# Kernel tuning notes

Hardware: AMD Instinct MI355X
Metric: run time of the kernel (lower is better)

Reference implementation:

```python
import jax, jax.numpy as jnp
import numpy as np

EPS = 1e-12

def _normalize(v):
    n = jnp.linalg.norm(v, axis=-1, keepdims=True)
    return v / jnp.maximum(n, EPS)

def _bgs(J):
    # J: [b, N, D, 3, 2] -> rotation matrices R [b, N, D, 3, 3]
    b1 = _normalize(J[..., :, 0])
    a2 = J[..., :, 1]
    dot = jnp.sum(b1 * a2, axis=-1, keepdims=True)
    b2 = _normalize(a2 - dot * b1)
    b3 = jnp.cross(b1, b2)
    return jnp.stack([b1, b2, b3], axis=-1)  # columns b1,b2,b3

def setup_inputs() -> dict:
    key = jax.random.key(0)
    k1, k2, k3, k4, k5 = jax.random.split(key, 5)
    B, N, D, OUT = 16, 4096, 64, 64
    X = jax.random.normal(k1, (B, N, D, 3), dtype=jnp.float32)
    J = jax.random.normal(k2, (B, N, D, 3, 2), dtype=jnp.float32)
    A = jax.random.normal(k3, (OUT, D), dtype=jnp.float32)
    Bm = jax.random.normal(k4, (OUT, D), dtype=jnp.float32)
    C = jax.random.normal(k5, (OUT, D), dtype=jnp.float32)
    return {"X": X, "J": J, "A": A, "Bm": Bm, "C": C}

def reference(X, J, A, Bm, C):
    R = _bgs(J)  # [b, N, D, 3, 3]
    # RT_i . X == column i of R dotted with X -> scalar per channel
    RTX = jnp.einsum('bndij,bndi->bndj', R, X)  # [b, N, D, 3], j-th entry = RT_j X
    rt0 = RTX[..., 0:1]
    rt1 = RTX[..., 1:2]
    rt2 = RTX[..., 2:3]
    col0 = R[..., :, 0]
    col1 = R[..., :, 1]
    col2 = R[..., :, 2]
    # a_term (after adding b_term, as in original forward)
    a_term = col1 * rt1 + col2 * rt2 + col2 * rt1 - col1 * rt2  # [b, N, D, 3]
    c_term = col0 * rt0
    Y = jnp.einsum('fe,bnei->bnfi', A, a_term) + jnp.einsum('fe,bnei->bnfi', C, c_term)
    Y = jnp.einsum('fe,bnei->bnfi', Bm, Y)
    return Y
```

## Files before the change

kernel.cpp:

```cpp
#include <hip/hip_runtime.h>


typedef __bf16 bf16x8 __attribute__((ext_vector_type(8)));
typedef float floatx4 __attribute__((ext_vector_type(4)));

#define ZRS  68
#define WLDS 816

__global__ __launch_bounds__(64) void prep_kernel(const float* __restrict__ A,
                                                  const float* __restrict__ Bm,
                                                  const float* __restrict__ C,
                                                  __bf16* __restrict__ acat) {
    int tid = blockIdx.x * 64 + threadIdx.x;
    int f = tid >> 6;
    int e = tid & 63;
    float m = 0.f, m2 = 0.f;
    #pragma unroll 8
    for (int k = 0; k < 64; ++k) {
        float b = Bm[f * 64 + k];
        m  = fmaf(b, A[k * 64 + e], m);
        m2 = fmaf(b, C[k * 64 + e], m2);
    }
    int mt  = f >> 4, l15 = f & 15;
    int k1  = 2 * e;
    int kc  = k1 >> 5;
    int qd  = (k1 >> 3) & 3;
    int j   = k1 & 7;
    int p   = ((mt * 4 + kc) * 64 + qd * 16 + l15) * 8 + j;
    acat[p]     = (__bf16)m;
    acat[p + 1] = (__bf16)m2;
}

static __device__ __forceinline__ unsigned pk(float a, float c) {
    unsigned short ua = __builtin_bit_cast(unsigned short, (__bf16)a);
    unsigned short uc = __builtin_bit_cast(unsigned short, (__bf16)c);
    return ((unsigned)uc << 16) | ua;
}

__global__ __launch_bounds__(256, 5) void main_kernel(const float* __restrict__ X,
                                                      const float* __restrict__ J,
                                                      const __bf16* __restrict__ acat,
                                                      float* __restrict__ out) {
    __shared__ __align__(16) float lds[4096 + 4 * WLDS];

    const int tid  = threadIdx.x;
    const int wave = tid >> 6;
    const int lane = tid & 63;
    const int l15  = lane & 15;
    const int quad = lane >> 4;
    const int pbase = blockIdx.x * 16 + wave * 4;

    const floatx4* ag = (const floatx4*)acat;
    floatx4 t0 = ag[tid];
    floatx4 t1 = ag[256 + tid];
    floatx4 t2 = ag[512 + tid];
    floatx4 t3 = ag[768 + tid];

    float2 jreg[4][3];
    float  xreg[4][3];
    {
        const float* Jb = J + (size_t)pbase * 384 + lane * 6;
        const float* Xb = X + (size_t)pbase * 192 + lane * 3;
        #pragma unroll
        for (int pi = 0; pi < 4; ++pi) {
            jreg[pi][0] = *(const float2*)(Jb + pi * 384);
            jreg[pi][1] = *(const float2*)(Jb + pi * 384 + 2);
            jreg[pi][2] = *(const float2*)(Jb + pi * 384 + 4);
            xreg[pi][0] = Xb[pi * 192];
            xreg[pi][1] = Xb[pi * 192 + 1];
            xreg[pi][2] = Xb[pi * 192 + 2];
        }
    }

    {
        floatx4* al = (floatx4*)lds;
        al[tid]       = t0;
        al[256 + tid] = t1;
        al[512 + tid] = t2;
        al[768 + tid] = t3;
    }

    float* zbase = lds + 4096 + wave * WLDS;

    #pragma unroll
    for (int pi = 0; pi < 4; ++pi) {
        float a0x = jreg[pi][0].x, a1x = jreg[pi][0].y;
        float a0y = jreg[pi][1].x, a1y = jreg[pi][1].y;
        float a0z = jreg[pi][2].x, a1z = jreg[pi][2].y;
        float xx = xreg[pi][0], xy = xreg[pi][1], xz = xreg[pi][2];

        float n0 = sqrtf(a0x * a0x + a0y * a0y + a0z * a0z);
        float r0 = 1.0f / fmaxf(n0, 1e-12f);
        float b1x = a0x * r0, b1y = a0y * r0, b1z = a0z * r0;

        float d  = b1x * a1x + b1y * a1y + b1z * a1z;
        float ux = a1x - d * b1x, uy = a1y - d * b1y, uz = a1z - d * b1z;
        float n2 = sqrtf(ux * ux + uy * uy + uz * uz);
        float r2 = 1.0f / fmaxf(n2, 1e-12f);
        float b2x = ux * r2, b2y = uy * r2, b2z = uz * r2;

        float b3x = b1y * b2z - b1z * b2y;
        float b3y = b1z * b2x - b1x * b2z;
        float b3z = b1x * b2y - b1y * b2x;

        float rt0 = b1x * xx + b1y * xy + b1z * xz;
        float rt1 = b2x * xx + b2y * xy + b2z * xz;
        float rt2 = b3x * xx + b3y * xy + b3z * xz;

        float s = rt1 - rt2, tt = rt1 + rt2;

        unsigned* zr = (unsigned*)zbase + pi * (3 * ZRS);
        zr[lane]           = pk(b2x * s + b3x * tt, b1x * rt0);
        zr[ZRS + lane]     = pk(b2y * s + b3y * tt, b1y * rt0);
        zr[2 * ZRS + lane] = pk(b2z * s + b3z * tt, b1z * rt0);
    }

    __syncthreads();

    floatx4 acc[4];
    #pragma unroll
    for (int mt = 0; mt < 4; ++mt) acc[mt] = (floatx4){0.f, 0.f, 0.f, 0.f};

    int row = l15 > 11 ? 11 : l15;
    int pz  = (row * 21846) >> 16;
    int iz  = row - pz * 3;
    const __bf16* zb   = (const __bf16*)zbase + pz * (3 * ZRS * 2) + iz * (ZRS * 2);
    const __bf16* albf = (const __bf16*)lds;
    #pragma unroll
    for (int kc = 0; kc < 4; ++kc) {
        bf16x8 b = *(const bf16x8*)(zb + kc * 32 + quad * 8);
        #pragma unroll
        for (int mt = 0; mt < 4; ++mt) {
            bf16x8 a = *(const bf16x8*)(albf + ((mt * 4 + kc) * 64 + lane) * 8);
            acc[mt] = __builtin_amdgcn_mfma_f32_16x16x32_bf16(a, b, acc[mt], 0, 0, 0);
        }
    }

    float* dl = zbase;
    #pragma unroll
    for (int mt = 0; mt < 4; ++mt) {
        int n = l15;
        if (n < 12) {
            int pl = (n * 21846) >> 16;
            int i  = n - pl * 3;
            float* dst = dl + pl * 196 + i;
            #pragma unroll
            for (int r = 0; r < 4; ++r) {
                int f = mt * 16 + quad * 4 + r;
                dst[f * 3] = acc[mt][r];
            }
        }
    }

    floatx4* og = (floatx4*)(out + (size_t)pbase * 192);
    #pragma unroll
    for (int t = 0; t < 3; ++t) {
        int g  = t * 64 + lane;
        int pg = (g * 1366) >> 16;
        int o  = g - pg * 48;
        og[g] = *(const floatx4*)(dl + pg * 196 + o * 4);
    }
}

extern "C" void kernel_launch(void* const* d_in, const int* in_sizes, int n_in,
                              void* d_out, int out_size, void* d_ws, size_t ws_size,
                              hipStream_t stream) {
    const float* X  = (const float*)d_in[0];
    const float* J  = (const float*)d_in[1];
    const float* A  = (const float*)d_in[2];
    const float* Bm = (const float*)d_in[3];
    const float* C  = (const float*)d_in[4];
    float* out = (float*)d_out;
    __bf16* acat = (__bf16*)d_ws;

    prep_kernel<<<64, 64, 0, stream>>>(A, Bm, C, acat);

    main_kernel<<<4096, 256, 0, stream>>>(X, J, acat, out);
}
```

Before: 205.7 us.

## Loop four point tiles per block with register prefetch of next J/X

Each block now processes four consecutive 16-point tiles, loading the next tile's J and X into registers while computing the current one. The grid shrinks by four and the staged weight matrix is loaded into LDS once per block instead of per tile. Launch bounds drop to 4 waves-occupancy hint to make room for the extra prefetch registers, and the per-wave LDS slab is slightly enlarged. The tradeoff is fewer resident blocks and less latency hiding from parallelism versus explicit software pipelining.

```diff
diff --git a/kernel.cpp b/kernel.cpp
--- a/kernel.cpp
+++ b/kernel.cpp
@@ -5,7 +5,7 @@
 typedef float floatx4 __attribute__((ext_vector_type(4)));
 
 #define ZRS  68
-#define WLDS 816
+#define WLDS 832
 
 __global__ __launch_bounds__(64) void prep_kernel(const float* __restrict__ A,
                                                   const float* __restrict__ Bm,
@@ -37,7 +37,7 @@
     return ((unsigned)uc << 16) | ua;
 }
 
-__global__ __launch_bounds__(256, 5) void main_kernel(const float* __restrict__ X,
+__global__ __launch_bounds__(256, 4) void main_kernel(const float* __restrict__ X,
                                                       const float* __restrict__ J,
                                                       const __bf16* __restrict__ acat,
                                                       float* __restrict__ out) {
@@ -48,7 +48,21 @@
     const int lane = tid & 63;
     const int l15  = lane & 15;
     const int quad = lane >> 4;
-    const int pbase = blockIdx.x * 16 + wave * 4;
+    const int bid  = blockIdx.x;
+
+    auto load_jx = [&](int pbase, float2 (&jr)[4][3], float (&xr)[4][3]) {
+        const float* Jb = J + (size_t)pbase * 384 + lane * 6;
+        const float* Xb = X + (size_t)pbase * 192 + lane * 3;
+        #pragma unroll
+        for (int pi = 0; pi < 4; ++pi) {
+            jr[pi][0] = *(const float2*)(Jb + pi * 384);
+            jr[pi][1] = *(const float2*)(Jb + pi * 384 + 2);
+            jr[pi][2] = *(const float2*)(Jb + pi * 384 + 4);
+            xr[pi][0] = Xb[pi * 192];
+            xr[pi][1] = Xb[pi * 192 + 1];
+            xr[pi][2] = Xb[pi * 192 + 2];
+        }
+    };
 
     const floatx4* ag = (const floatx4*)acat;
     floatx4 t0 = ag[tid];
@@ -56,21 +70,8 @@
     floatx4 t2 = ag[512 + tid];
     floatx4 t3 = ag[768 + tid];
 
-    float2 jreg[4][3];
-    float  xreg[4][3];
-    {
-        const float* Jb = J + (size_t)pbase * 384 + lane * 6;
-        const float* Xb = X + (size_t)pbase * 192 + lane * 3;
-        #pragma unroll
-        for (int pi = 0; pi < 4; ++pi) {
-            jreg[pi][0] = *(const float2*)(Jb + pi * 384);
-            jreg[pi][1] = *(const float2*)(Jb + pi * 384 + 2);
-            jreg[pi][2] = *(const float2*)(Jb + pi * 384 + 4);
-            xreg[pi][0] = Xb[pi * 192];
-            xreg[pi][1] = Xb[pi * 192 + 1];
-            xreg[pi][2] = Xb[pi * 192 + 2];
-        }
-    }
+    float2 jcur[4][3]; float xcur[4][3];
+    load_jx(bid * 64 + wave * 4, jcur, xcur);
 
     {
         floatx4* al = (floatx4*)lds;
@@ -79,86 +80,106 @@
         al[512 + tid] = t2;
         al[768 + tid] = t3;
     }
+    __syncthreads();
 
     float* zbase = lds + 4096 + wave * WLDS;
+    const __bf16* albf = (const __bf16*)lds;
 
     #pragma unroll
-    for (int pi = 0; pi < 4; ++pi) {
-        float a0x = jreg[pi][0].x, a1x = jreg[pi][0].y;
-        float a0y = jreg[pi][1].x, a1y = jreg[pi][1].y;
-        float a0z = jreg[pi][2].x, a1z = jreg[pi][2].y;
-        float xx = xreg[pi][0], xy = xreg[pi][1], xz = xreg[pi][2];
-
-        float n0 = sqrtf(a0x * a0x + a0y * a0y + a0z * a0z);
-        float r0 = 1.0f / fmaxf(n0, 1e-12f);
-        float b1x = a0x * r0, b1y = a0y * r0, b1z = a0z * r0;
-
-        float d  = b1x * a1x + b1y * a1y + b1z * a1z;
-        float ux = a1x - d * b1x, uy = a1y - d * b1y, uz = a1z - d * b1z;
-        float n2 = sqrtf(ux * ux + uy * uy + uz * uz);
-        float r2 = 1.0f / fmaxf(n2, 1e-12f);
-        float b2x = ux * r2, b2y = uy * r2, b2z = uz * r2;
-
-        float b3x = b1y * b2z - b1z * b2y;
-        float b3y = b1z * b2x - b1x * b2z;
-        float b3z = b1x * b2y - b1y * b2x;
-
-        float rt0 = b1x * xx + b1y * xy + b1z * xz;
-        float rt1 = b2x * xx + b2y * xy + b2z * xz;
-        float rt2 = b3x * xx + b3y * xy + b3z * xz;
-
-        float s = rt1 - rt2, tt = rt1 + rt2;
-
-        unsigned* zr = (unsigned*)zbase + pi * (3 * ZRS);
-        zr[lane]           = pk(b2x * s + b3x * tt, b1x * rt0);
-        zr[ZRS + lane]     = pk(b2y * s + b3y * tt, b1y * rt0);
-        zr[2 * ZRS + lane] = pk(b2z * s + b3z * tt, b1z * rt0);
-    }
-
-    __syncthreads();
-
-    floatx4 acc[4];
-    #pragma unroll
-    for (int mt = 0; mt < 4; ++mt) acc[mt] = (floatx4){0.f, 0.f, 0.f, 0.f};
-
-    int row = l15 > 11 ? 11 : l15;
-    int pz  = (row * 21846) >> 16;
-    int iz  = row - pz * 3;
-    const __bf16* zb   = (const __bf16*)zbase + pz * (3 * ZRS * 2) + iz * (ZRS * 2);
-    const __bf16* albf = (const __bf16*)lds;
-    #pragma unroll
-    for (int kc = 0; kc < 4; ++kc) {
-        bf16x8 b = *(const bf16x8*)(zb + kc * 32 + quad * 8);
+    for (int it = 0; it < 4; ++it) {
+        const int pbase = bid * 64 + it * 16 + wave * 4;
+
+        float2 jnxt[4][3]; float xnxt[4][3];
+        if (it < 3) load_jx(pbase + 16, jnxt, xnxt);
+        __builtin_amdgcn_sched_barrier(0);
+
+        #pragma unroll
+        for (int pi = 0; pi < 4; ++pi) {
+            float a0x = jcur[pi][0].x, a1x = jcur[pi][0].y;
+            float a0y = jcur[pi][1].x, a1y = jcur[pi][1].y;
+            float a0z = jcur[pi][2].x, a1z = jcur[pi][2].y;
+            float xx = xcur[pi][0], xy = xcur[pi][1], xz = xcur[pi][2];
+
+            float n0 = sqrtf(a0x * a0x + a0y * a0y + a0z * a0z);
+            float r0 = 1.0f / fmaxf(n0, 1e-12f);
+            float b1x = a0x * r0, b1y = a0y * r0, b1z = a0z * r0;
+
+            float d  = b1x * a1x + b1y * a1y + b1z * a1z;
+            float ux = a1x - d * b1x, uy = a1y - d * b1y, uz = a1z - d * b1z;
+            float n2 = sqrtf(ux * ux + uy * uy + uz * uz);
+            float r2 = 1.0f / fmaxf(n2, 1e-12f);
+            float b2x = ux * r2, b2y = uy * r2, b2z = uz * r2;
+
+            float b3x = b1y * b2z - b1z * b2y;
+            float b3y = b1z * b2x - b1x * b2z;
+            float b3z = b1x * b2y - b1y * b2x;
+
+            float rt0 = b1x * xx + b1y * xy + b1z * xz;
+            float rt1 = b2x * xx + b2y * xy + b2z * xz;
+            float rt2 = b3x * xx + b3y * xy + b3z * xz;
+
+            float s = rt1 - rt2, tt = rt1 + rt2;
+
+            unsigned* zr = (unsigned*)zbase + pi * (3 * ZRS);
+            zr[lane]           = pk(b2x * s + b3x * tt, b1x * rt0);
+            zr[ZRS + lane]     = pk(b2y * s + b3y * tt, b1y * rt0);
+            zr[2 * ZRS + lane] = pk(b2z * s + b3z * tt, b1z * rt0);
+        }
+
+        floatx4 acc[4];
+        #pragma unroll
+        for (int mt = 0; mt < 4; ++mt) acc[mt] = (floatx4){0.f, 0.f, 0.f, 0.f};
+
+        int row = l15 > 11 ? 11 : l15;
+        int pz  = (row * 21846) >> 16;
+        int iz  = row - pz * 3;
+        const __bf16* zb = (const __bf16*)zbase + pz * (3 * ZRS * 2) + iz * (ZRS * 2);
+        #pragma unroll
+        for (int kc = 0; kc < 4; ++kc) {
+            bf16x8 b = *(const bf16x8*)(zb + kc * 32 + quad * 8);
+            #pragma unroll
+            for (int mt = 0; mt < 4; ++mt) {
+                bf16x8 a = *(const bf16x8*)(albf + ((mt * 4 + kc) * 64 + lane) * 8);
+                acc[mt] = __builtin_amdgcn_mfma_f32_16x16x32_bf16(a, b, acc[mt], 0, 0, 0);
+            }
+        }
+
+        float* dl = zbase;
         #pragma unroll
         for (int mt = 0; mt < 4; ++mt) {
-            bf16x8 a = *(const bf16x8*)(albf + ((mt * 4 + kc) * 64 + lane) * 8);
-            acc[mt] = __builtin_amdgcn_mfma_f32_16x16x32_bf16(a, b, acc[mt], 0, 0, 0);
-        }
-    }
-
-    float* dl = zbase;
-    #pragma unroll
-    for (int mt = 0; mt < 4; ++mt) {
-        int n = l15;
-        if (n < 12) {
-            int pl = (n * 21846) >> 16;
-            int i  = n - pl * 3;
-            float* dst = dl + pl * 196 + i;
+            int n = l15;
+            if (n < 12) {
+                int pl = (n * 21846) >> 16;
+                int i  = n - pl * 3;
+                float* dst = dl + pl * 196 + i;
+                #pragma unroll
+                for (int r = 0; r < 4; ++r) {
+                    int f = mt * 16 + quad * 4 + r;
+                    dst[f * 3] = acc[mt][r];
+                }
+            }
+        }
+
+        floatx4* og = (floatx4*)(out + (size_t)pbase * 192);
+        #pragma unroll
+        for (int t = 0; t < 3; ++t) {
+            int g  = t * 64 + lane;
+            int pg = (g * 1366) >> 16;
+            int o  = g - pg * 48;
+            og[g] = *(const floatx4*)(dl + pg * 196 + o * 4);
+        }
+
+        if (it < 3) {
             #pragma unroll
-            for (int r = 0; r < 4; ++r) {
-                int f = mt * 16 + quad * 4 + r;
-                dst[f * 3] = acc[mt][r];
+            for (int pi = 0; pi < 4; ++pi) {
+                jcur[pi][0] = jnxt[pi][0];
+                jcur[pi][1] = jnxt[pi][1];
+                jcur[pi][2] = jnxt[pi][2];
+                xcur[pi][0] = xnxt[pi][0];
+                xcur[pi][1] = xnxt[pi][1];
+                xcur[pi][2] = xnxt[pi][2];
             }
         }
-    }
-
-    floatx4* og = (floatx4*)(out + (size_t)pbase * 192);
-    #pragma unroll
-    for (int t = 0; t < 3; ++t) {
-        int g  = t * 64 + lane;
-        int pg = (g * 1366) >> 16;
-        int o  = g - pg * 48;
-        og[g] = *(const floatx4*)(dl + pg * 196 + o * 4);
     }
 }
 
@@ -175,5 +196,5 @@
 
     prep_kernel<<<64, 64, 0, stream>>>(A, Bm, C, acat);
 
-    main_kernel<<<4096, 256, 0, stream>>>(X, J, acat, out);
-}
+    main_kernel<<<1024, 256, 0, stream>>>(X, J, acat, out);
+}
```

Result: slower. 210.5 us (+2.4%).

## Make main kernel persistent with double-buffered global-to-LDS async loads

Applied to the files above, without the earlier changes.

Each wave now processes 8 tiles of 4 points in a loop instead of one tile per block. The next tile's J and X are prefetched directly into LDS with global_load_lds and double buffering, paced by manual vmcnt waits. The A-fragment weights are held in registers rather than staged through shared memory, and the launch shrinks to 512 blocks. This aims to overlap memory latency with compute and to amortize the weight loads, but it lowers occupancy (launch bounds 2) and relies on hand-counted waitcnt values and per-wave buffer reuse without block-level barriers.

```diff
diff --git a/kernel.cpp b/kernel.cpp
--- a/kernel.cpp
+++ b/kernel.cpp
@@ -4,8 +4,7 @@
 typedef __bf16 bf16x8 __attribute__((ext_vector_type(8)));
 typedef float floatx4 __attribute__((ext_vector_type(4)));
 
-#define ZRS  68
-#define WLDS 816
+#define ZRS 68
 
 __global__ __launch_bounds__(64) void prep_kernel(const float* __restrict__ A,
                                                   const float* __restrict__ Bm,
@@ -37,128 +36,144 @@
     return ((unsigned)uc << 16) | ua;
 }
 
-__global__ __launch_bounds__(256, 5) void main_kernel(const float* __restrict__ X,
+static __device__ __forceinline__ void glds16(const float* g, float* l) {
+    __builtin_amdgcn_global_load_lds(
+        (const __attribute__((address_space(1))) void*)g,
+        (__attribute__((address_space(3))) void*)l, 16, 0, 0);
+}
+
+__global__ __launch_bounds__(256, 2) void main_kernel(const float* __restrict__ X,
                                                       const float* __restrict__ J,
                                                       const __bf16* __restrict__ acat,
                                                       float* __restrict__ out) {
-    __shared__ __align__(16) float lds[4096 + 4 * WLDS];
+    __shared__ __align__(16) float lds[4 * 2 * 2304];
 
     const int tid  = threadIdx.x;
     const int wave = tid >> 6;
     const int lane = tid & 63;
     const int l15  = lane & 15;
     const int quad = lane >> 4;
-    const int pbase = blockIdx.x * 16 + wave * 4;
+    const size_t pw0 = ((size_t)blockIdx.x * 4 + wave) * 32;
 
-    const floatx4* ag = (const floatx4*)acat;
-    floatx4 t0 = ag[tid];
-    floatx4 t1 = ag[256 + tid];
-    floatx4 t2 = ag[512 + tid];
-    floatx4 t3 = ag[768 + tid];
+    float* buf0 = lds + wave * 4608;
+    float* buf1 = buf0 + 2304;
 
-    float2 jreg[4][3];
-    float  xreg[4][3];
-    {
-        const float* Jb = J + (size_t)pbase * 384 + lane * 6;
-        const float* Xb = X + (size_t)pbase * 192 + lane * 3;
+    bf16x8 afrag[4][4];
+    #pragma unroll
+    for (int mt = 0; mt < 4; ++mt)
+        #pragma unroll
+        for (int kc = 0; kc < 4; ++kc)
+            afrag[mt][kc] = *(const bf16x8*)(acat + ((mt * 4 + kc) * 64 + lane) * 8);
+
+    auto stage = [&](int tile, float* dst) {
+        const float* jg = J + (pw0 + tile * 4) * 384 + lane * 4;
+        const float* xg = X + (pw0 + tile * 4) * 192 + lane * 4;
+        #pragma unroll
+        for (int u = 0; u < 6; ++u) glds16(jg + u * 256, dst + u * 256);
+        #pragma unroll
+        for (int u = 0; u < 3; ++u) glds16(xg + u * 256, dst + 1536 + u * 256);
+    };
+
+    stage(0, buf0);
+
+    #pragma unroll 2
+    for (int t = 0; t < 8; ++t) {
+        float* cur = (t & 1) ? buf1 : buf0;
+        float* nxt = (t & 1) ? buf0 : buf1;
+
+        if (t < 7) stage(t + 1, nxt);
+
+        if (t == 0)      asm volatile("s_waitcnt vmcnt(9)" ::: "memory");
+        else if (t == 7) asm volatile("s_waitcnt vmcnt(3)" ::: "memory");
+        else             asm volatile("s_waitcnt vmcnt(12)" ::: "memory");
+
+        float2 jr[4][3];
+        float  xr[4][3];
         #pragma unroll
         for (int pi = 0; pi < 4; ++pi) {
-            jreg[pi][0] = *(const float2*)(Jb + pi * 384);
-            jreg[pi][1] = *(const float2*)(Jb + pi * 384 + 2);
-            jreg[pi][2] = *(const float2*)(Jb + pi * 384 + 4);
-            xreg[pi][0] = Xb[pi * 192];
-            xreg[pi][1] = Xb[pi * 192 + 1];
-            xreg[pi][2] = Xb[pi * 192 + 2];
+            const float* jst = cur + pi * 384 + lane * 6;
+            jr[pi][0] = *(const float2*)(jst);
+            jr[pi][1] = *(const float2*)(jst + 2);
+            jr[pi][2] = *(const float2*)(jst + 4);
+            const float* xst = cur + 1536 + pi * 192 + lane * 3;
+            xr[pi][0] = xst[0]; xr[pi][1] = xst[1]; xr[pi][2] = xst[2];
         }
-    }
 
-    {
-        floatx4* al = (floatx4*)lds;
-        al[tid]       = t0;
-        al[256 + tid] = t1;
-        al[512 + tid] = t2;
-        al[768 + tid] = t3;
-    }
+        #pragma unroll
+        for (int pi = 0; pi < 4; ++pi) {
+            float a0x = jr[pi][0].x, a1x = jr[pi][0].y;
+            float a0y = jr[pi][1].x, a1y = jr[pi][1].y;
+            float a0z = jr[pi][2].x, a1z = jr[pi][2].y;
+            float xx = xr[pi][0], xy = xr[pi][1], xz = xr[pi][2];
 
-    float* zbase = lds + 4096 + wave * WLDS;
+            float n0 = sqrtf(a0x * a0x + a0y * a0y + a0z * a0z);
+            float r0 = 1.0f / fmaxf(n0, 1e-12f);
+            float b1x = a0x * r0, b1y = a0y * r0, b1z = a0z * r0;
 
-    #pragma unroll
-    for (int pi = 0; pi < 4; ++pi) {
-        float a0x = jreg[pi][0].x, a1x = jreg[pi][0].y;
-        float a0y = jreg[pi][1].x, a1y = jreg[pi][1].y;
-        float a0z = jreg[pi][2].x, a1z = jreg[pi][2].y;
-        float xx = xreg[pi][0], xy = xreg[pi][1], xz = xreg[pi][2];
+            float d  = b1x * a1x + b1y * a1y + b1z * a1z;
+            float ux = a1x - d * b1x, uy = a1y - d * b1y, uz = a1z - d * b1z;
+            float n2 = sqrtf(ux * ux + uy * uy + uz * uz);
+            float r2 = 1.0f / fmaxf(n2, 1e-12f);
+            float b2x = ux * r2, b2y = uy * r2, b2z = uz * r2;
 
-        float n0 = sqrtf(a0x * a0x + a0y * a0y + a0z * a0z);
-        float r0 = 1.0f / fmaxf(n0, 1e-12f);
-        float b1x = a0x * r0, b1y = a0y * r0, b1z = a0z * r0;
+            float b3x = b1y * b2z - b1z * b2y;
+            float b3y = b1z * b2x - b1x * b2z;
+            float b3z = b1x * b2y - b1y * b2x;
 
-        float d  = b1x * a1x + b1y * a1y + b1z * a1z;
-        float ux = a1x - d * b1x, uy = a1y - d * b1y, uz = a1z - d * b1z;
-        float n2 = sqrtf(ux * ux + uy * uy + uz * uz);
-        float r2 = 1.0f / fmaxf(n2, 1e-12f);
-        float b2x = ux * r2, b2y = uy * r2, b2z = uz * r2;
+            float rt0 = b1x * xx + b1y * xy + b1z * xz;
+            float rt1 = b2x * xx + b2y * xy + b2z * xz;
+            float rt2 = b3x * xx + b3y * xy + b3z * xz;
 
-        float b3x = b1y * b2z - b1z * b2y;
-        float b3y = b1z * b2x - b1x * b2z;
-        float b3z = b1x * b2y - b1y * b2x;
+            float s = rt1 - rt2, tt = rt1 + rt2;
 
-        float rt0 = b1x * xx + b1y * xy + b1z * xz;
-        float rt1 = b2x * xx + b2y * xy + b2z * xz;
-        float rt2 = b3x * xx + b3y * xy + b3z * xz;
+            unsigned* zr = (unsigned*)cur + pi * (3 * ZRS);
+            zr[lane]           = pk(b2x * s + b3x * tt, b1x * rt0);
+            zr[ZRS + lane]     = pk(b2y * s + b3y * tt, b1y * rt0);
+            zr[2 * ZRS + lane] = pk(b2z * s + b3z * tt, b1z * rt0);
+        }
 
-        float s = rt1 - rt2, tt = rt1 + rt2;
+        floatx4 acc[4];
+        #pragma unroll
+        for (int mt = 0; mt < 4; ++mt) acc[mt] = (floatx4){0.f, 0.f, 0.f, 0.f};
 
-        unsigned* zr = (unsigned*)zbase + pi * (3 * ZRS);
-        zr[lane]           = pk(b2x * s + b3x * tt, b1x * rt0);
-        zr[ZRS + lane]     = pk(b2y * s + b3y * tt, b1y * rt0);
-        zr[2 * ZRS + lane] = pk(b2z * s + b3z * tt, b1z * rt0);
-    }
+        int row = l15 > 11 ? 11 : l15;
+        int pz  = (row * 21846) >> 16;
+        int iz  = row - pz * 3;
+        const __bf16* zb = (const __bf16*)cur + pz * (3 * ZRS * 2) + iz * (ZRS * 2);
+        #pragma unroll
+        for (int kc = 0; kc < 4; ++kc) {
+            bf16x8 b = *(const bf16x8*)(zb + kc * 32 + quad * 8);
+            #pragma unroll
+            for (int mt = 0; mt < 4; ++mt)
+                acc[mt] = __builtin_amdgcn_mfma_f32_16x16x32_bf16(afrag[mt][kc], b, acc[mt], 0, 0, 0);
+        }
 
-    __syncthreads();
-
-    floatx4 acc[4];
-    #pragma unroll
-    for (int mt = 0; mt < 4; ++mt) acc[mt] = (floatx4){0.f, 0.f, 0.f, 0.f};
-
-    int row = l15 > 11 ? 11 : l15;
-    int pz  = (row * 21846) >> 16;
-    int iz  = row - pz * 3;
-    const __bf16* zb   = (const __bf16*)zbase + pz * (3 * ZRS * 2) + iz * (ZRS * 2);
-    const __bf16* albf = (const __bf16*)lds;
-    #pragma unroll
-    for (int kc = 0; kc < 4; ++kc) {
-        bf16x8 b = *(const bf16x8*)(zb + kc * 32 + quad * 8);
+        float* dl = cur;
         #pragma unroll
         for (int mt = 0; mt < 4; ++mt) {
-            bf16x8 a = *(const bf16x8*)(albf + ((mt * 4 + kc) * 64 + lane) * 8);
-            acc[mt] = __builtin_amdgcn_mfma_f32_16x16x32_bf16(a, b, acc[mt], 0, 0, 0);
-        }
-    }
-
-    float* dl = zbase;
-    #pragma unroll
-    for (int mt = 0; mt < 4; ++mt) {
-        int n = l15;
-        if (n < 12) {
-            int pl = (n * 21846) >> 16;
-            int i  = n - pl * 3;
-            float* dst = dl + pl * 196 + i;
-            #pragma unroll
-            for (int r = 0; r < 4; ++r) {
-                int f = mt * 16 + quad * 4 + r;
-                dst[f * 3] = acc[mt][r];
+            int n = l15;
+            if (n < 12) {
+                int pl = (n * 21846) >> 16;
+                int i  = n - pl * 3;
+                float* dst = dl + pl * 196 + i;
+                #pragma unroll
+                for (int r = 0; r < 4; ++r) {
+                    int f = mt * 16 + quad * 4 + r;
+                    dst[f * 3] = acc[mt][r];
+                }
             }
         }
-    }
 
-    floatx4* og = (floatx4*)(out + (size_t)pbase * 192);
-    #pragma unroll
-    for (int t = 0; t < 3; ++t) {
-        int g  = t * 64 + lane;
-        int pg = (g * 1366) >> 16;
-        int o  = g - pg * 48;
-        og[g] = *(const floatx4*)(dl + pg * 196 + o * 4);
+        floatx4* og = (floatx4*)(out + (pw0 + t * 4) * 192);
+        #pragma unroll
+        for (int u = 0; u < 3; ++u) {
+            int g  = u * 64 + lane;
+            int pg = (g * 1366) >> 16;
+            int o  = g - pg * 48;
+            og[g] = *(const floatx4*)(dl + pg * 196 + o * 4);
+        }
+
+        asm volatile("s_waitcnt lgkmcnt(0)" ::: "memory");
     }
 }
 
@@ -175,5 +190,5 @@
 
     prep_kernel<<<64, 64, 0, stream>>>(A, Bm, C, acat);
 
-    main_kernel<<<4096, 256, 0, stream>>>(X, J, acat, out);
+    main_kernel<<<512, 256, 0, stream>>>(X, J, acat, out);
 }
```

Measured after the change: 216.0 us. 5.0% more time.
